# Optimization experiments

Hardware: AMD Instinct MI355X
Metric: run time of the kernel (lower is better)

Reference implementation:

```python
import jax, jax.numpy as jnp
import numpy as np

NH, NKV, HD = 32, 8, 64  # num heads, num kv heads, head_dim


def apply_rope(x, fc):
    # x: [B,S,H,D], fc: [S, D//2, 2]
    b, s, h, d = x.shape
    xr = x.reshape(b, s, h, d // 2, 2)
    fc = fc.reshape(1, s, 1, d // 2, 2)
    out = jnp.stack([
        xr[..., 0] * fc[..., 0] - xr[..., 1] * fc[..., 1],
        xr[..., 1] * fc[..., 0] + xr[..., 0] * fc[..., 1],
    ], axis=-1)
    return out.reshape(b, s, h, d)


def setup_inputs() -> dict:
    key = jax.random.key(0)
    k0, k1, k2 = jax.random.split(key, 3)
    B, S, H = 1, 2048, 2048
    x = jax.random.normal(k0, (B, S, H), jnp.float32)
    # rotary cos/sin table: [S, HD//2, 2]
    pos = jnp.arange(S, dtype=jnp.float32)
    inv_freq = 1.0 / (10000.0 ** (jnp.arange(0, HD, 2, dtype=jnp.float32) / HD))
    ang = pos[:, None] * inv_freq[None, :]
    freqs_cis = jnp.stack([jnp.cos(ang), jnp.sin(ang)], axis=-1)
    # causal bool mask [1,1,S,S]
    mask = jnp.tril(jnp.ones((S, S), dtype=bool))[None, None]
    scale = H ** -0.5
    Wqkv = jax.random.normal(k1, ((NH + 2 * NKV) * HD, H), jnp.float32) * scale
    Wo = jax.random.normal(k2, (H, H), jnp.float32) * scale
    return {"x": x, "freqs_cis": freqs_cis, "mask": mask, "Wqkv": Wqkv, "Wo": Wo}


def reference(x, freqs_cis, mask, Wqkv, Wo):
    B, S, H = x.shape
    g = NH // NKV  # GQA group size
    qkv = x @ Wqkv.T  # [B,S,(NH+2*NKV)*HD]
    q, k, v = jnp.split(qkv, [NH * HD, NH * HD + NKV * HD], axis=-1)
    q = q.reshape(B, S, NH, HD)
    k = k.reshape(B, S, NKV, HD)
    v = v.reshape(B, S, NKV, HD)
    q = apply_rope(q, freqs_cis)
    k = apply_rope(k, freqs_cis)
    # group query heads by shared kv head instead of repeat_interleave on K/V
    q = q.reshape(B, S, NKV, g, HD)
    scores = jnp.einsum('bskgd,btkd->bkgst', q, k) * (HD ** -0.5)
    scores = jnp.where(mask.reshape(1, 1, 1, S, S), scores, -jnp.inf)
    p = jax.nn.softmax(scores, axis=-1)
    y = jnp.einsum('bkgst,btkd->bskgd', p, v).reshape(B, S, H)
    return y @ Wo.T
```

## Files before the change

kernel.cpp:

```cpp
#include <hip/hip_runtime.h>
#include <stdint.h>

typedef unsigned short ushort_t;
typedef __attribute__((ext_vector_type(8))) short s8v;
typedef __attribute__((ext_vector_type(4))) float f4v;

#define NH 32
#define NKV 8
#define HD 64
#define S_LEN 2048
#define HID 2048
#define DQKV 3072

#define QSCALE 0.18033688011112042f

__device__ __forceinline__ ushort_t f2b(float f) {
  union { float f; unsigned u; } v; v.f = f;
  unsigned r = v.u + 0x7FFFu + ((v.u >> 16) & 1u);
  return (ushort_t)(r >> 16);
}
__device__ __forceinline__ float b2f(ushort_t h) {
  union { unsigned u; float f; } v; v.u = ((unsigned)h) << 16;
  return v.f;
}
__device__ __forceinline__ unsigned pkbf(float lo, float hi) {
  return ((unsigned)f2b(hi) << 16) | (unsigned)f2b(lo);
}

__global__ void cvt_bf16(const float* __restrict__ in, ushort_t* __restrict__ out, int n4) {
  int stride = gridDim.x * blockDim.x;
  for (int i = blockIdx.x * blockDim.x + threadIdx.x; i < n4; i += stride) {
    float4 v = ((const float4*)in)[i];
    uint2 p;
    p.x = (unsigned)f2b(v.x) | ((unsigned)f2b(v.y) << 16);
    p.y = (unsigned)f2b(v.z) | ((unsigned)f2b(v.w) << 16);
    ((uint2*)out)[i] = p;
  }
}

template <typename CT>
__global__ __launch_bounds__(256) void gemm_bt(
    const ushort_t* __restrict__ A, const ushort_t* __restrict__ B,
    CT* __restrict__ C, int M, int N, int K) {
  __shared__ ushort_t sA[128 * 32];
  __shared__ ushort_t sB[128 * 32];
  const int tid = threadIdx.x;
  const int wave = tid >> 6, lane = tid & 63;
  const int bm = blockIdx.y * 128, bn = blockIdx.x * 128;
  const int wm = (wave >> 1) * 64, wn = (wave & 1) * 64;
  const int srow = wave * 16 + (lane >> 2);
  const int scol = (lane & 3) * 8;
  const int fr = lane & 15, fg = lane >> 4;

  f4v acc[4][4];
#pragma unroll
  for (int m = 0; m < 4; ++m)
#pragma unroll
    for (int n = 0; n < 4; ++n) acc[m][n] = (f4v){0.f, 0.f, 0.f, 0.f};

  for (int k0 = 0; k0 < K; k0 += 32) {
    __syncthreads();
#pragma unroll
    for (int it = 0; it < 2; ++it) {
      int r = it * 64 + srow;
      __builtin_amdgcn_global_load_lds(
          (const __attribute__((address_space(1))) void*)(A + (size_t)(bm + r) * K + k0 + scol),
          (__attribute__((address_space(3))) void*)(&sA[(it * 64 + wave * 16) * 32]),
          16, 0, 0);
      __builtin_amdgcn_global_load_lds(
          (const __attribute__((address_space(1))) void*)(B + (size_t)(bn + r) * K + k0 + scol),
          (__attribute__((address_space(3))) void*)(&sB[(it * 64 + wave * 16) * 32]),
          16, 0, 0);
    }
    __syncthreads();

    s8v af[4], bf[4];
#pragma unroll
    for (int m = 0; m < 4; ++m)
      af[m] = *(const s8v*)&sA[(wm + m * 16 + fr) * 32 + fg * 8];
#pragma unroll
    for (int n = 0; n < 4; ++n)
      bf[n] = *(const s8v*)&sB[(wn + n * 16 + fr) * 32 + fg * 8];
#pragma unroll
    for (int m = 0; m < 4; ++m)
#pragma unroll
      for (int n = 0; n < 4; ++n)
        acc[m][n] = __builtin_amdgcn_mfma_f32_16x16x32_bf16(af[m], bf[n], acc[m][n], 0, 0, 0);
  }

#pragma unroll
  for (int m = 0; m < 4; ++m)
#pragma unroll
    for (int n = 0; n < 4; ++n)
#pragma unroll
      for (int rr = 0; rr < 4; ++rr) {
        int row = bm + wm + m * 16 + fg * 4 + rr;
        int col = bn + wn + n * 16 + fr;
        float v = acc[m][n][rr];
        if constexpr (sizeof(CT) == 2)
          C[(size_t)row * N + col] = (CT)f2b(v);
        else
          C[(size_t)row * N + col] = v;
      }
}

__global__ void rope_qk(const ushort_t* __restrict__ qkv, const float* __restrict__ fc,
                        ushort_t* __restrict__ Qb, ushort_t* __restrict__ Kb) {
  int tid = blockIdx.x * blockDim.x + threadIdx.x;
  if (tid >= S_LEN * 160) return;
  int s = tid / 160, c = tid - s * 160;
  int h = c >> 2, part = c & 3;
  const ushort_t* src = qkv + (size_t)s * DQKV + h * 64 + part * 16;
  s8v va = *(const s8v*)src;
  s8v vb = *(const s8v*)(src + 8);
  const float* fp = fc + s * 64 + part * 16;
  float4 f0 = ((const float4*)fp)[0];
  float4 f1 = ((const float4*)fp)[1];
  float4 f2 = ((const float4*)fp)[2];
  float4 f3 = ((const float4*)fp)[3];
  float cs[8] = {f0.x, f0.z, f1.x, f1.z, f2.x, f2.z, f3.x, f3.z};
  float sn[8] = {f0.y, f0.w, f1.y, f1.w, f2.y, f2.w, f3.y, f3.w};
  const float scale = (h < NH) ? QSCALE : 1.0f;
  ushort_t ob[16];
#pragma unroll
  for (int i = 0; i < 8; ++i) {
    float x0, x1;
    if (i < 4) { x0 = b2f((ushort_t)va[2 * i]); x1 = b2f((ushort_t)va[2 * i + 1]); }
    else       { x0 = b2f((ushort_t)vb[2 * i - 8]); x1 = b2f((ushort_t)vb[2 * i - 7]); }
    float o0 = (x0 * cs[i] - x1 * sn[i]) * scale;
    float o1 = (x1 * cs[i] + x0 * sn[i]) * scale;
    ob[2 * i] = f2b(o0);
    ob[2 * i + 1] = f2b(o1);
  }
  ushort_t* dst;
  if (h < NH) dst = Qb + ((size_t)s * NH + h) * 64 + part * 16;
  else        dst = Kb + ((size_t)s * NKV + (h - NH)) * 64 + part * 16;
  *(s8v*)dst = *(const s8v*)&ob[0];
  *(s8v*)(dst + 8) = *(const s8v*)&ob[8];
}

__global__ void transp_v(const ushort_t* __restrict__ qkv, ushort_t* __restrict__ Vt) {
  __shared__ ushort_t t[32][33];
  int hd0 = blockIdx.x * 32, s0 = blockIdx.y * 32;
#pragma unroll
  for (int k = 0; k < 4; ++k) {
    int sy = threadIdx.y + k * 8;
    t[sy][threadIdx.x] = qkv[(size_t)(s0 + sy) * DQKV + 2560 + hd0 + threadIdx.x];
  }
  __syncthreads();
#pragma unroll
  for (int k = 0; k < 4; ++k) {
    int hy = threadIdx.y + k * 8;
    Vt[(size_t)(hd0 + hy) * S_LEN + s0 + threadIdx.x] = t[threadIdx.x][hy];
  }
}

__global__ __launch_bounds__(64) void attn(
    const ushort_t* __restrict__ Q, const ushort_t* __restrict__ Kc,
    const ushort_t* __restrict__ Vt, ushort_t* __restrict__ Y) {
  const int head = blockIdx.y, kvh = head >> 2;
  const int lane = threadIdx.x;
  const int fr = lane & 15, fg = lane >> 4;

#pragma unroll
  for (int half = 0; half < 2; ++half) {
    const int j = half ? (127 - (int)blockIdx.x) : (int)blockIdx.x;
    const int q0 = j * 16;

    s8v qf[2];
#pragma unroll
    for (int c = 0; c < 2; ++c)
      qf[c] = *(const s8v*)(Q + ((size_t)(q0 + fr) * NH + head) * 64 + c * 32 + fg * 8);

    float m = -3.0e38f, l = 0.f;
    f4v yacc[4];
#pragma unroll
    for (int d = 0; d < 4; ++d) yacc[d] = (f4v){0.f, 0.f, 0.f, 0.f};

    const int ntiles = q0 / 64 + 1;
    for (int t = 0; t < ntiles; ++t) {
      const int kv0 = t * 64;
      f4v sc[4];
#pragma unroll
      for (int n = 0; n < 4; ++n) {
        const int krow = kv0 + 32 * (n >> 1) + 8 * (fr >> 2) + 4 * (n & 1) + (fr & 3);
        f4v a = (f4v){0.f, 0.f, 0.f, 0.f};
#pragma unroll
        for (int c = 0; c < 2; ++c) {
          s8v kf = *(const s8v*)(Kc + ((size_t)krow * NKV + kvh) * 64 + c * 32 + fg * 8);
          a = __builtin_amdgcn_mfma_f32_16x16x32_bf16(kf, qf[c], a, 0, 0, 0);
        }
        sc[n] = a;
      }
      if (t == ntiles - 1) {
#pragma unroll
        for (int n = 0; n < 4; ++n)
#pragma unroll
          for (int r = 0; r < 4; ++r) {
            int kv = kv0 + 32 * (n >> 1) + 8 * fg + 4 * (n & 1) + r;
            if (kv > q0 + fr) sc[n][r] = -1e30f;
          }
      }
      float pmax = sc[0][0];
#pragma unroll
      for (int n = 0; n < 4; ++n)
#pragma unroll
        for (int r = 0; r < 4; ++r) pmax = fmaxf(pmax, sc[n][r]);
      pmax = fmaxf(pmax, __shfl_xor(pmax, 16));
      pmax = fmaxf(pmax, __shfl_xor(pmax, 32));
      if (!__all(pmax <= m + 8.f)) {
        float mn = fmaxf(m, pmax);
        float al = exp2f(m - mn);
        m = mn;
        l *= al;
        float aly[4];
#pragma unroll
        for (int rr = 0; rr < 4; ++rr) aly[rr] = __shfl(al, fg * 4 + rr);
#pragma unroll
        for (int d = 0; d < 4; ++d)
#pragma unroll
          for (int rr = 0; rr < 4; ++rr) yacc[d][rr] *= aly[rr];
      }
      float rs = 0.f;
#pragma unroll
      for (int n = 0; n < 4; ++n)
#pragma unroll
        for (int r = 0; r < 4; ++r) {
          float p = exp2f(sc[n][r] - m);
          sc[n][r] = p;
          rs += p;
        }
      rs += __shfl_xor(rs, 16);
      rs += __shfl_xor(rs, 32);
      l += rs;
      s8v pf[2];
#pragma unroll
      for (int c = 0; c < 2; ++c) {
        unsigned w0 = pkbf(sc[2 * c][0], sc[2 * c][1]);
        unsigned w1 = pkbf(sc[2 * c][2], sc[2 * c][3]);
        unsigned w2 = pkbf(sc[2 * c + 1][0], sc[2 * c + 1][1]);
        unsigned w3 = pkbf(sc[2 * c + 1][2], sc[2 * c + 1][3]);
        unsigned wb[4] = {w0, w1, w2, w3};
        pf[c] = *(const s8v*)&wb[0];
      }
#pragma unroll
      for (int d = 0; d < 4; ++d) {
#pragma unroll
        for (int c = 0; c < 2; ++c) {
          s8v vf = *(const s8v*)(Vt + (size_t)(kvh * 64 + d * 16 + fr) * S_LEN + kv0 + c * 32 + fg * 8);
          yacc[d] = __builtin_amdgcn_mfma_f32_16x16x32_bf16(pf[c], vf, yacc[d], 0, 0, 0);
        }
      }
    }
    float linv[4];
#pragma unroll
    for (int rr = 0; rr < 4; ++rr) linv[rr] = 1.f / __shfl(l, fg * 4 + rr);
#pragma unroll
    for (int d = 0; d < 4; ++d)
#pragma unroll
      for (int rr = 0; rr < 4; ++rr) {
        float v = yacc[d][rr] * linv[rr];
        Y[(size_t)(q0 + fg * 4 + rr) * HID + head * 64 + d * 16 + fr] = f2b(v);
      }
  }
}

extern "C" void kernel_launch(void* const* d_in, const int* in_sizes, int n_in,
                              void* d_out, int out_size, void* d_ws, size_t ws_size,
                              hipStream_t stream) {
  const float* x    = (const float*)d_in[0];
  const float* fc   = (const float*)d_in[1];
  const float* wqkv = (const float*)d_in[3];
  const float* wo   = (const float*)d_in[4];
  float* out = (float*)d_out;

  char* ws = (char*)d_ws;
  ushort_t* xb    = (ushort_t*)(ws);
  ushort_t* wqkvb = (ushort_t*)(ws + 8388608);
  ushort_t* wob   = (ushort_t*)(ws + 20971520);
  ushort_t* qkvb  = (ushort_t*)(ws + 29360128);
  ushort_t* Qb    = (ushort_t*)(ws + 41943040);
  ushort_t* Kb    = (ushort_t*)(ws + 50331648);
  ushort_t* Vtb   = (ushort_t*)(ws + 52428800);
  ushort_t* Yb    = xb;

  cvt_bf16<<<4096, 256, 0, stream>>>(x, xb, 1048576);
  cvt_bf16<<<4096, 256, 0, stream>>>(wqkv, wqkvb, 1572864);
  cvt_bf16<<<4096, 256, 0, stream>>>(wo, wob, 1048576);

  gemm_bt<ushort_t><<<dim3(24, 16), 256, 0, stream>>>(xb, wqkvb, qkvb, 2048, 3072, 2048);

  rope_qk<<<1280, 256, 0, stream>>>(qkvb, fc, Qb, Kb);
  transp_v<<<dim3(16, 64), dim3(32, 8), 0, stream>>>(qkvb, Vtb);

  attn<<<dim3(64, 32), 64, 0, stream>>>(Qb, Kb, Vtb, Yb);

  gemm_bt<float><<<dim3(16, 16), 256, 0, stream>>>(Yb, wob, out, 2048, 2048, 2048);
}
```

Before: 341.0 us.

## Split-K GEMMs with atomics, fuse converts, interleave attention query blocks

```diff
diff --git a/kernel.cpp b/kernel.cpp
--- a/kernel.cpp
+++ b/kernel.cpp
@@ -19,29 +19,31 @@
   unsigned r = v.u + 0x7FFFu + ((v.u >> 16) & 1u);
   return (ushort_t)(r >> 16);
 }
-__device__ __forceinline__ float b2f(ushort_t h) {
-  union { unsigned u; float f; } v; v.u = ((unsigned)h) << 16;
-  return v.f;
-}
-__device__ __forceinline__ unsigned pkbf(float lo, float hi) {
-  return ((unsigned)f2b(hi) << 16) | (unsigned)f2b(lo);
-}
-
-__global__ void cvt_bf16(const float* __restrict__ in, ushort_t* __restrict__ out, int n4) {
-  int stride = gridDim.x * blockDim.x;
-  for (int i = blockIdx.x * blockDim.x + threadIdx.x; i < n4; i += stride) {
-    float4 v = ((const float4*)in)[i];
-    uint2 p;
-    p.x = (unsigned)f2b(v.x) | ((unsigned)f2b(v.y) << 16);
-    p.y = (unsigned)f2b(v.z) | ((unsigned)f2b(v.w) << 16);
-    ((uint2*)out)[i] = p;
-  }
-}
-
-template <typename CT>
-__global__ __launch_bounds__(256) void gemm_bt(
+__device__ __forceinline__ unsigned cvtpk(float lo, float hi) {
+  unsigned r;
+  asm("v_cvt_pk_bf16_f32 %0, %1, %2" : "=v"(r) : "v"(lo), "v"(hi));
+  return r;
+}
+
+__global__ void cvt3(const float* __restrict__ a, const float* __restrict__ b,
+                     const float* __restrict__ c, ushort_t* __restrict__ oa,
+                     ushort_t* __restrict__ ob, ushort_t* __restrict__ oc) {
+  const int n1 = 1048576, n2 = 1572864;
+  int i = blockIdx.x * blockDim.x + threadIdx.x;
+  const float* in; ushort_t* out; int j;
+  if (i < n1) { in = a; out = oa; j = i; }
+  else if (i < n1 + n2) { in = b; out = ob; j = i - n1; }
+  else { in = c; out = oc; j = i - n1 - n2; }
+  float4 v = ((const float4*)in)[j];
+  uint2 p;
+  p.x = cvtpk(v.x, v.y);
+  p.y = cvtpk(v.z, v.w);
+  ((uint2*)out)[j] = p;
+}
+
+__global__ __launch_bounds__(256) void gemm_bt_sk(
     const ushort_t* __restrict__ A, const ushort_t* __restrict__ B,
-    CT* __restrict__ C, int M, int N, int K) {
+    float* __restrict__ C, int M, int N, int K) {
   __shared__ ushort_t sA[128 * 32];
   __shared__ ushort_t sB[128 * 32];
   const int tid = threadIdx.x;
@@ -51,6 +53,8 @@
   const int srow = wave * 16 + (lane >> 2);
   const int scol = (lane & 3) * 8;
   const int fr = lane & 15, fg = lane >> 4;
+  const int khalf = K >> 1;
+  const int kbeg = blockIdx.z * khalf;
 
   f4v acc[4][4];
 #pragma unroll
@@ -58,7 +62,7 @@
 #pragma unroll
     for (int n = 0; n < 4; ++n) acc[m][n] = (f4v){0.f, 0.f, 0.f, 0.f};
 
-  for (int k0 = 0; k0 < K; k0 += 32) {
+  for (int k0 = kbeg; k0 < kbeg + khalf; k0 += 32) {
     __syncthreads();
 #pragma unroll
     for (int it = 0; it < 2; ++it) {
@@ -96,63 +100,116 @@
       for (int rr = 0; rr < 4; ++rr) {
         int row = bm + wm + m * 16 + fg * 4 + rr;
         int col = bn + wn + n * 16 + fr;
-        float v = acc[m][n][rr];
-        if constexpr (sizeof(CT) == 2)
-          C[(size_t)row * N + col] = (CT)f2b(v);
-        else
-          C[(size_t)row * N + col] = v;
+        unsafeAtomicAdd(&C[(size_t)row * N + col], acc[m][n][rr]);
       }
 }
 
-__global__ void rope_qk(const ushort_t* __restrict__ qkv, const float* __restrict__ fc,
+__global__ void rope_qk(const float* __restrict__ qkvF, const float* __restrict__ fc,
                         ushort_t* __restrict__ Qb, ushort_t* __restrict__ Kb) {
   int tid = blockIdx.x * blockDim.x + threadIdx.x;
   if (tid >= S_LEN * 160) return;
   int s = tid / 160, c = tid - s * 160;
   int h = c >> 2, part = c & 3;
-  const ushort_t* src = qkv + (size_t)s * DQKV + h * 64 + part * 16;
-  s8v va = *(const s8v*)src;
-  s8v vb = *(const s8v*)(src + 8);
+  const float* src = qkvF + (size_t)s * DQKV + h * 64 + part * 16;
+  float xv[16];
+  ((float4*)xv)[0] = ((const float4*)src)[0];
+  ((float4*)xv)[1] = ((const float4*)src)[1];
+  ((float4*)xv)[2] = ((const float4*)src)[2];
+  ((float4*)xv)[3] = ((const float4*)src)[3];
   const float* fp = fc + s * 64 + part * 16;
-  float4 f0 = ((const float4*)fp)[0];
-  float4 f1 = ((const float4*)fp)[1];
-  float4 f2 = ((const float4*)fp)[2];
-  float4 f3 = ((const float4*)fp)[3];
-  float cs[8] = {f0.x, f0.z, f1.x, f1.z, f2.x, f2.z, f3.x, f3.z};
-  float sn[8] = {f0.y, f0.w, f1.y, f1.w, f2.y, f2.w, f3.y, f3.w};
+  float fv[16];
+  ((float4*)fv)[0] = ((const float4*)fp)[0];
+  ((float4*)fv)[1] = ((const float4*)fp)[1];
+  ((float4*)fv)[2] = ((const float4*)fp)[2];
+  ((float4*)fv)[3] = ((const float4*)fp)[3];
   const float scale = (h < NH) ? QSCALE : 1.0f;
-  ushort_t ob[16];
+  ushort_t obuf[16];
 #pragma unroll
   for (int i = 0; i < 8; ++i) {
-    float x0, x1;
-    if (i < 4) { x0 = b2f((ushort_t)va[2 * i]); x1 = b2f((ushort_t)va[2 * i + 1]); }
-    else       { x0 = b2f((ushort_t)vb[2 * i - 8]); x1 = b2f((ushort_t)vb[2 * i - 7]); }
-    float o0 = (x0 * cs[i] - x1 * sn[i]) * scale;
-    float o1 = (x1 * cs[i] + x0 * sn[i]) * scale;
-    ob[2 * i] = f2b(o0);
-    ob[2 * i + 1] = f2b(o1);
+    float x0 = xv[2 * i], x1 = xv[2 * i + 1];
+    float cs = fv[2 * i], sn = fv[2 * i + 1];
+    obuf[2 * i]     = f2b((x0 * cs - x1 * sn) * scale);
+    obuf[2 * i + 1] = f2b((x1 * cs + x0 * sn) * scale);
   }
   ushort_t* dst;
   if (h < NH) dst = Qb + ((size_t)s * NH + h) * 64 + part * 16;
   else        dst = Kb + ((size_t)s * NKV + (h - NH)) * 64 + part * 16;
-  *(s8v*)dst = *(const s8v*)&ob[0];
-  *(s8v*)(dst + 8) = *(const s8v*)&ob[8];
-}
-
-__global__ void transp_v(const ushort_t* __restrict__ qkv, ushort_t* __restrict__ Vt) {
-  __shared__ ushort_t t[32][33];
+  *(s8v*)dst = *(const s8v*)&obuf[0];
+  *(s8v*)(dst + 8) = *(const s8v*)&obuf[8];
+}
+
+__global__ void transp_v(const float* __restrict__ qkvF, ushort_t* __restrict__ Vt) {
+  __shared__ float t[32][33];
   int hd0 = blockIdx.x * 32, s0 = blockIdx.y * 32;
 #pragma unroll
   for (int k = 0; k < 4; ++k) {
     int sy = threadIdx.y + k * 8;
-    t[sy][threadIdx.x] = qkv[(size_t)(s0 + sy) * DQKV + 2560 + hd0 + threadIdx.x];
+    t[sy][threadIdx.x] = qkvF[(size_t)(s0 + sy) * DQKV + 2560 + hd0 + threadIdx.x];
   }
   __syncthreads();
 #pragma unroll
   for (int k = 0; k < 4; ++k) {
     int hy = threadIdx.y + k * 8;
-    Vt[(size_t)(hd0 + hy) * S_LEN + s0 + threadIdx.x] = t[threadIdx.x][hy];
-  }
+    Vt[(size_t)(hd0 + hy) * S_LEN + s0 + threadIdx.x] = f2b(t[threadIdx.x][hy]);
+  }
+}
+
+__device__ __forceinline__ void softmax_pack(f4v (&sc)[4], float& m, float& l,
+                                             f4v (&y)[4], s8v (&pf)[2], int fg) {
+  float pmax = sc[0][0];
+#pragma unroll
+  for (int n = 0; n < 4; ++n)
+#pragma unroll
+    for (int r = 0; r < 4; ++r) pmax = fmaxf(pmax, sc[n][r]);
+  pmax = fmaxf(pmax, __shfl_xor(pmax, 16));
+  pmax = fmaxf(pmax, __shfl_xor(pmax, 32));
+  if (!__all(pmax <= m + 8.f)) {
+    float mn = fmaxf(m, pmax);
+    float al = exp2f(m - mn);
+    m = mn;
+    l *= al;
+    float aly[4];
+#pragma unroll
+    for (int rr = 0; rr < 4; ++rr) aly[rr] = __shfl(al, fg * 4 + rr);
+#pragma unroll
+    for (int d = 0; d < 4; ++d)
+#pragma unroll
+      for (int rr = 0; rr < 4; ++rr) y[d][rr] *= aly[rr];
+  }
+  float rs = 0.f;
+#pragma unroll
+  for (int n = 0; n < 4; ++n)
+#pragma unroll
+    for (int r = 0; r < 4; ++r) {
+      float p = exp2f(sc[n][r] - m);
+      sc[n][r] = p;
+      rs += p;
+    }
+  l += rs;
+#pragma unroll
+  for (int c = 0; c < 2; ++c) {
+    unsigned wb[4];
+    wb[0] = cvtpk(sc[2 * c][0], sc[2 * c][1]);
+    wb[1] = cvtpk(sc[2 * c][2], sc[2 * c][3]);
+    wb[2] = cvtpk(sc[2 * c + 1][0], sc[2 * c + 1][1]);
+    wb[3] = cvtpk(sc[2 * c + 1][2], sc[2 * c + 1][3]);
+    pf[c] = *(const s8v*)&wb[0];
+  }
+}
+
+__device__ __forceinline__ void finalize_y(f4v (&y)[4], float l, int q0, int head,
+                                           int fr, int fg, ushort_t* __restrict__ Y) {
+  l += __shfl_xor(l, 16);
+  l += __shfl_xor(l, 32);
+  float linv[4];
+#pragma unroll
+  for (int rr = 0; rr < 4; ++rr) linv[rr] = 1.f / __shfl(l, fg * 4 + rr);
+#pragma unroll
+  for (int d = 0; d < 4; ++d)
+#pragma unroll
+    for (int rr = 0; rr < 4; ++rr)
+      Y[(size_t)(q0 + fg * 4 + rr) * HID + head * 64 + d * 16 + fr] =
+          f2b(y[d][rr] * linv[rr]);
 }
 
 __global__ __launch_bounds__(64) void attn(
@@ -161,108 +218,90 @@
   const int head = blockIdx.y, kvh = head >> 2;
   const int lane = threadIdx.x;
   const int fr = lane & 15, fg = lane >> 4;
-
-#pragma unroll
-  for (int half = 0; half < 2; ++half) {
-    const int j = half ? (127 - (int)blockIdx.x) : (int)blockIdx.x;
-    const int q0 = j * 16;
-
-    s8v qf[2];
-#pragma unroll
-    for (int c = 0; c < 2; ++c)
-      qf[c] = *(const s8v*)(Q + ((size_t)(q0 + fr) * NH + head) * 64 + c * 32 + fg * 8);
-
-    float m = -3.0e38f, l = 0.f;
-    f4v yacc[4];
-#pragma unroll
-    for (int d = 0; d < 4; ++d) yacc[d] = (f4v){0.f, 0.f, 0.f, 0.f};
-
-    const int ntiles = q0 / 64 + 1;
-    for (int t = 0; t < ntiles; ++t) {
-      const int kv0 = t * 64;
-      f4v sc[4];
+  const int jA = 127 - (int)blockIdx.x;
+  const int jB = (int)blockIdx.x;
+  const int q0A = jA * 16, q0B = jB * 16;
+  const int ntA = (q0A >> 6) + 1, ntB = (q0B >> 6) + 1;
+
+  s8v qfA[2], qfB[2];
+#pragma unroll
+  for (int c = 0; c < 2; ++c) {
+    qfA[c] = *(const s8v*)(Q + ((size_t)(q0A + fr) * NH + head) * 64 + c * 32 + fg * 8);
+    qfB[c] = *(const s8v*)(Q + ((size_t)(q0B + fr) * NH + head) * 64 + c * 32 + fg * 8);
+  }
+
+  float mA = -3.0e38f, lA = 0.f, mB = -3.0e38f, lB = 0.f;
+  f4v yA[4], yB[4];
+#pragma unroll
+  for (int d = 0; d < 4; ++d) {
+    yA[d] = (f4v){0.f, 0.f, 0.f, 0.f};
+    yB[d] = (f4v){0.f, 0.f, 0.f, 0.f};
+  }
+
+  for (int t = 0; t < ntA; ++t) {
+    const int kv0 = t * 64;
+    const bool doB = (t < ntB);
+    s8v kf[4][2];
+#pragma unroll
+    for (int n = 0; n < 4; ++n) {
+      const int krow = kv0 + 32 * (n >> 1) + 8 * (fr >> 2) + 4 * (n & 1) + (fr & 3);
+      const ushort_t* kb = Kc + ((size_t)krow * NKV + kvh) * 64 + fg * 8;
+      kf[n][0] = *(const s8v*)kb;
+      kf[n][1] = *(const s8v*)(kb + 32);
+    }
+    f4v scA[4], scB[4];
+#pragma unroll
+    for (int n = 0; n < 4; ++n) {
+      f4v a = (f4v){0.f, 0.f, 0.f, 0.f};
+      a = __builtin_amdgcn_mfma_f32_16x16x32_bf16(kf[n][0], qfA[0], a, 0, 0, 0);
+      a = __builtin_amdgcn_mfma_f32_16x16x32_bf16(kf[n][1], qfA[1], a, 0, 0, 0);
+      scA[n] = a;
+    }
+    if (doB) {
 #pragma unroll
       for (int n = 0; n < 4; ++n) {
-        const int krow = kv0 + 32 * (n >> 1) + 8 * (fr >> 2) + 4 * (n & 1) + (fr & 3);
         f4v a = (f4v){0.f, 0.f, 0.f, 0.f};
-#pragma unroll
-        for (int c = 0; c < 2; ++c) {
-          s8v kf = *(const s8v*)(Kc + ((size_t)krow * NKV + kvh) * 64 + c * 32 + fg * 8);
-          a = __builtin_amdgcn_mfma_f32_16x16x32_bf16(kf, qf[c], a, 0, 0, 0);
+        a = __builtin_amdgcn_mfma_f32_16x16x32_bf16(kf[n][0], qfB[0], a, 0, 0, 0);
+        a = __builtin_amdgcn_mfma_f32_16x16x32_bf16(kf[n][1], qfB[1], a, 0, 0, 0);
+        scB[n] = a;
+      }
+    }
+    if (t == ntA - 1) {
+#pragma unroll
+      for (int n = 0; n < 4; ++n)
+#pragma unroll
+        for (int r = 0; r < 4; ++r) {
+          int kv = kv0 + 32 * (n >> 1) + 8 * fg + 4 * (n & 1) + r;
+          if (kv > q0A + fr) scA[n][r] = -1e30f;
         }
-        sc[n] = a;
+    }
+    if (doB && t == ntB - 1) {
+#pragma unroll
+      for (int n = 0; n < 4; ++n)
+#pragma unroll
+        for (int r = 0; r < 4; ++r) {
+          int kv = kv0 + 32 * (n >> 1) + 8 * fg + 4 * (n & 1) + r;
+          if (kv > q0B + fr) scB[n][r] = -1e30f;
+        }
+    }
+    s8v pfA[2], pfB[2];
+    softmax_pack(scA, mA, lA, yA, pfA, fg);
+    if (doB) softmax_pack(scB, mB, lB, yB, pfB, fg);
+#pragma unroll
+    for (int d = 0; d < 4; ++d) {
+      const ushort_t* vb = Vt + ((size_t)(kvh * 64 + d * 16 + fr)) * S_LEN + kv0 + fg * 8;
+      s8v vf0 = *(const s8v*)vb;
+      s8v vf1 = *(const s8v*)(vb + 32);
+      yA[d] = __builtin_amdgcn_mfma_f32_16x16x32_bf16(pfA[0], vf0, yA[d], 0, 0, 0);
+      yA[d] = __builtin_amdgcn_mfma_f32_16x16x32_bf16(pfA[1], vf1, yA[d], 0, 0, 0);
+      if (doB) {
+        yB[d] = __builtin_amdgcn_mfma_f32_16x16x32_bf16(pfB[0], vf0, yB[d], 0, 0, 0);
+        yB[d] = __builtin_amdgcn_mfma_f32_16x16x32_bf16(pfB[1], vf1, yB[d], 0, 0, 0);
       }
-      if (t == ntiles - 1) {
-#pragma unroll
-        for (int n = 0; n < 4; ++n)
-#pragma unroll
-          for (int r = 0; r < 4; ++r) {
-            int kv = kv0 + 32 * (n >> 1) + 8 * fg + 4 * (n & 1) + r;
-            if (kv > q0 + fr) sc[n][r] = -1e30f;
-          }
-      }
-      float pmax = sc[0][0];
-#pragma unroll
-      for (int n = 0; n < 4; ++n)
-#pragma unroll
-        for (int r = 0; r < 4; ++r) pmax = fmaxf(pmax, sc[n][r]);
-      pmax = fmaxf(pmax, __shfl_xor(pmax, 16));
-      pmax = fmaxf(pmax, __shfl_xor(pmax, 32));
-      if (!__all(pmax <= m + 8.f)) {
-        float mn = fmaxf(m, pmax);
-        float al = exp2f(m - mn);
-        m = mn;
-        l *= al;
-        float aly[4];
-#pragma unroll
-        for (int rr = 0; rr < 4; ++rr) aly[rr] = __shfl(al, fg * 4 + rr);
-#pragma unroll
-        for (int d = 0; d < 4; ++d)
-#pragma unroll
-          for (int rr = 0; rr < 4; ++rr) yacc[d][rr] *= aly[rr];
-      }
-      float rs = 0.f;
-#pragma unroll
-      for (int n = 0; n < 4; ++n)
-#pragma unroll
-        for (int r = 0; r < 4; ++r) {
-          float p = exp2f(sc[n][r] - m);
-          sc[n][r] = p;
-          rs += p;
-        }
-      rs += __shfl_xor(rs, 16);
-      rs += __shfl_xor(rs, 32);
-      l += rs;
-      s8v pf[2];
-#pragma unroll
-      for (int c = 0; c < 2; ++c) {
-        unsigned w0 = pkbf(sc[2 * c][0], sc[2 * c][1]);
-        unsigned w1 = pkbf(sc[2 * c][2], sc[2 * c][3]);
-        unsigned w2 = pkbf(sc[2 * c + 1][0], sc[2 * c + 1][1]);
-        unsigned w3 = pkbf(sc[2 * c + 1][2], sc[2 * c + 1][3]);
-        unsigned wb[4] = {w0, w1, w2, w3};
-        pf[c] = *(const s8v*)&wb[0];
-      }
-#pragma unroll
-      for (int d = 0; d < 4; ++d) {
-#pragma unroll
-        for (int c = 0; c < 2; ++c) {
-          s8v vf = *(const s8v*)(Vt + (size_t)(kvh * 64 + d * 16 + fr) * S_LEN + kv0 + c * 32 + fg * 8);
-          yacc[d] = __builtin_amdgcn_mfma_f32_16x16x32_bf16(pf[c], vf, yacc[d], 0, 0, 0);
-        }
-      }
-    }
-    float linv[4];
-#pragma unroll
-    for (int rr = 0; rr < 4; ++rr) linv[rr] = 1.f / __shfl(l, fg * 4 + rr);
-#pragma unroll
-    for (int d = 0; d < 4; ++d)
-#pragma unroll
-      for (int rr = 0; rr < 4; ++rr) {
-        float v = yacc[d][rr] * linv[rr];
-        Y[(size_t)(q0 + fg * 4 + rr) * HID + head * 64 + d * 16 + fr] = f2b(v);
-      }
-  }
+    }
+  }
+  finalize_y(yA, lA, q0A, head, fr, fg, Y);
+  finalize_y(yB, lB, q0B, head, fr, fg, Y);
 }
 
 extern "C" void kernel_launch(void* const* d_in, const int* in_sizes, int n_in,
@@ -277,23 +316,24 @@
   char* ws = (char*)d_ws;
   ushort_t* xb    = (ushort_t*)(ws);
   ushort_t* wqkvb = (ushort_t*)(ws + 8388608);
+  ushort_t* Qb    = (ushort_t*)(ws + 8388608);
+  ushort_t* Kb    = (ushort_t*)(ws + 16777216);
+  ushort_t* Vtb   = (ushort_t*)(ws + 18874368);
   ushort_t* wob   = (ushort_t*)(ws + 20971520);
-  ushort_t* qkvb  = (ushort_t*)(ws + 29360128);
-  ushort_t* Qb    = (ushort_t*)(ws + 41943040);
-  ushort_t* Kb    = (ushort_t*)(ws + 50331648);
-  ushort_t* Vtb   = (ushort_t*)(ws + 52428800);
+  float*    qkvF  = (float*)(ws + 29360128);
   ushort_t* Yb    = xb;
 
-  cvt_bf16<<<4096, 256, 0, stream>>>(x, xb, 1048576);
-  cvt_bf16<<<4096, 256, 0, stream>>>(wqkv, wqkvb, 1572864);
-  cvt_bf16<<<4096, 256, 0, stream>>>(wo, wob, 1048576);
-
-  gemm_bt<ushort_t><<<dim3(24, 16), 256, 0, stream>>>(xb, wqkvb, qkvb, 2048, 3072, 2048);
-
-  rope_qk<<<1280, 256, 0, stream>>>(qkvb, fc, Qb, Kb);
-  transp_v<<<dim3(16, 64), dim3(32, 8), 0, stream>>>(qkvb, Vtb);
+  hipMemsetAsync(qkvF, 0, 25165824, stream);
+  hipMemsetAsync(out, 0, 16777216, stream);
+
+  cvt3<<<14336, 256, 0, stream>>>(x, wqkv, wo, xb, wqkvb, wob);
+
+  gemm_bt_sk<<<dim3(24, 16, 2), 256, 0, stream>>>(xb, wqkvb, qkvF, 2048, 3072, 2048);
+
+  rope_qk<<<1280, 256, 0, stream>>>(qkvF, fc, Qb, Kb);
+  transp_v<<<dim3(16, 64), dim3(32, 8), 0, stream>>>(qkvF, Vtb);
 
   attn<<<dim3(64, 32), 64, 0, stream>>>(Qb, Kb, Vtb, Yb);
 
-  gemm_bt<float><<<dim3(16, 16), 256, 0, stream>>>(Yb, wob, out, 2048, 2048, 2048);
-}
+  gemm_bt_sk<<<dim3(16, 16, 2), 256, 0, stream>>>(Yb, wob, out, 2048, 2048, 2048);
+}
```

Result: slower. 363.5 us (+6.6%).
